# Performance work log

Hardware: AMD Instinct MI355X
Metric: run time of the kernel (lower is better)

The kernel has to match this reference:

```python
import jax, jax.numpy as jnp
import numpy as np

# MLA dims (DeepSeek-V3-lite style)
B, S, DIM = 1, 2048, 2048
H, NOPE, ROPE, VD, LORA = 16, 128, 64, 128, 512
QK_HEAD = NOPE + ROPE  # 192
SCALE = QK_HEAD ** -0.5
EPS = 1e-6


def _rmsnorm(x, w):
    return x * jax.lax.rsqrt(jnp.mean(x * x, axis=-1, keepdims=True) + EPS) * w


def _apply_rope(x, cos, sin):
    # x: [b, s, h, d] with interleaved (real, imag) pairs; cos/sin: [s, d//2]
    x0, x1 = x[..., 0::2], x[..., 1::2]
    c = cos[None, :, None, :]
    s = sin[None, :, None, :]
    y0 = x0 * c - x1 * s
    y1 = x0 * s + x1 * c
    return jnp.stack([y0, y1], axis=-1).reshape(x.shape)


def setup_inputs() -> dict:
    key = jax.random.key(0)
    ks = jax.random.split(key, 6)
    x = jax.random.normal(ks[0], (B, S, DIM), jnp.float32) * 0.02
    wq = jax.random.normal(ks[1], (H * QK_HEAD, DIM), jnp.float32) * 0.02
    wkv_a = jax.random.normal(ks[2], (LORA + ROPE, DIM), jnp.float32) * 0.02
    kv_norm_w = jnp.ones((LORA,), jnp.float32)
    wkv_b = jax.random.normal(ks[3], (H * (NOPE + VD), LORA), jnp.float32) * 0.02
    wo = jax.random.normal(ks[4], (DIM, H * VD), jnp.float32) * 0.02
    # rotary freqs_cis (cos/sin) for qk_rope_head_dim
    inv_freq = 1.0 / (10000.0 ** (np.arange(0, ROPE, 2, dtype=np.float32) / ROPE))
    t = np.arange(S, dtype=np.float32)
    ang = np.outer(t, inv_freq)  # [S, ROPE//2]
    cos = jnp.asarray(np.cos(ang), jnp.float32)
    sin = jnp.asarray(np.sin(ang), jnp.float32)
    return {"x": x, "cos": cos, "sin": sin, "wq": wq, "wkv_a": wkv_a,
            "kv_norm_w": kv_norm_w, "wkv_b": wkv_b, "wo": wo}


def reference(x, cos, sin, wq, wkv_a, kv_norm_w, wkv_b, wo):
    b, s, _ = x.shape
    # queries
    q = (x @ wq.T).reshape(b, s, H, QK_HEAD)
    q_nope, q_pe = q[..., :NOPE], q[..., NOPE:]
    q_pe = _apply_rope(q_pe, cos, sin)  # [b,s,h,rope]
    # latent kv
    kv = x @ wkv_a.T  # [b,s,lora+rope]
    kv_c, k_pe = kv[..., :LORA], kv[..., LORA:]
    k_pe = _apply_rope(k_pe[:, :, None, :], cos, sin)[:, :, 0, :]  # [b,s,rope]
    kv_c = _rmsnorm(kv_c, kv_norm_w)  # latent kv cache [b,s,lora]
    # absorbed weights: wkv_b viewed as [h, nope+vd, lora]
    wkv_b_r = wkv_b.reshape(H, NOPE + VD, LORA)
    w_uk = wkv_b_r[:, :NOPE]   # [h, nope, lora]
    w_uv = wkv_b_r[:, NOPE:]   # [h, vd, lora]
    # absorb: project q_nope into latent space
    q_c = jnp.einsum('bshd,hdc->bshc', q_nope, w_uk)  # [b,s,h,lora]
    scores = (jnp.einsum('bshc,btc->bsht', q_c, kv_c)
              + jnp.einsum('bshr,btr->bsht', q_pe, k_pe)) * SCALE
    # causal mask over [s, t]
    mask = jnp.where(jnp.arange(s)[:, None] >= jnp.arange(s)[None, :], 0.0, -1e30)
    scores = scores + mask[None, :, None, :].astype(scores.dtype)
    attn = jax.nn.softmax(scores, axis=-1)
    o = jnp.einsum('bsht,btc->bshc', attn, kv_c)       # [b,s,h,lora]
    o = jnp.einsum('bshc,hdc->bshd', o, w_uv)           # [b,s,h,vd]
    out = o.reshape(b, s, H * VD) @ wo.T                # [b,s,dim]
    return out
```

## Files before the change

### kernel.cpp

```cpp
#include <hip/hip_runtime.h>
#include <hip/hip_bf16.h>
#include <math.h>

#define S_LEN 2048
#define DIM   2048
#define H_N   16
#define NOPE  128
#define ROPE  64
#define VD    128
#define LORA  512
#define D_QK  576
#define SCALE_F 0.07216878364870323f
#define EPS_F 1e-6f
#define KVF 640
#define KVS 1280

typedef short short8 __attribute__((ext_vector_type(8)));
typedef short short4v __attribute__((ext_vector_type(4)));
typedef float floatx4 __attribute__((ext_vector_type(4)));

static __device__ inline unsigned short f2bf_bits(float f) {
  union { __hip_bfloat16 h; unsigned short u; } cv;
  cv.h = __float2bfloat16(f);
  return cv.u;
}

static __device__ inline float bf2f(unsigned short b) {
  union { unsigned u; float f; } cv;
  cv.u = (unsigned)b << 16;
  return cv.f;
}

static __device__ inline void gload_lds16(const short* gptr, short* lds_base_uniform) {
  __builtin_amdgcn_global_load_lds(
      (const __attribute__((address_space(1))) void*)gptr,
      (__attribute__((address_space(3))) void*)lds_base_uniform, 16, 0, 0);
}

__global__ __launch_bounds__(256) void cast_f32_bf16(
    const float* __restrict__ src, short* __restrict__ dst, int n8) {
  int i = blockIdx.x * 256 + threadIdx.x;
  if (i < n8) {
    float4 a = ((const float4*)src)[2 * i];
    float4 b = ((const float4*)src)[2 * i + 1];
    uint4 o;
    o.x = (unsigned)f2bf_bits(a.x) | ((unsigned)f2bf_bits(a.y) << 16);
    o.y = (unsigned)f2bf_bits(a.z) | ((unsigned)f2bf_bits(a.w) << 16);
    o.z = (unsigned)f2bf_bits(b.x) | ((unsigned)f2bf_bits(b.y) << 16);
    o.w = (unsigned)f2bf_bits(b.z) | ((unsigned)f2bf_bits(b.w) << 16);
    ((uint4*)dst)[i] = o;
  }
}

__global__ __launch_bounds__(256) void zero_short8(short* __restrict__ dst, int n8) {
  int i = blockIdx.x * 256 + threadIdx.x;
  if (i < n8) ((uint4*)dst)[i] = (uint4){0u, 0u, 0u, 0u};
}

__global__ __launch_bounds__(256) void transpose_wuk(
    const float* __restrict__ wkvb, short* __restrict__ wukT) {
  __shared__ float tile[32][33];
  const int h = blockIdx.z, c0 = blockIdx.y * 32, d0 = blockIdx.x * 32;
  const int t = threadIdx.x;
  const int r = t >> 3, c4 = (t & 7) * 4;
  float4 v = *(const float4*)(wkvb + ((long)h * 256 + d0 + r) * 512 + c0 + c4);
  tile[r][c4 + 0] = v.x; tile[r][c4 + 1] = v.y;
  tile[r][c4 + 2] = v.z; tile[r][c4 + 3] = v.w;
  __syncthreads();
  uint2 o;
  o.x = (unsigned)f2bf_bits(tile[c4 + 0][r]) | ((unsigned)f2bf_bits(tile[c4 + 1][r]) << 16);
  o.y = (unsigned)f2bf_bits(tile[c4 + 2][r]) | ((unsigned)f2bf_bits(tile[c4 + 3][r]) << 16);
  *(uint2*)(wukT + ((long)h * 512 + c0 + r) * 128 + d0 + c4) = o;
}

__global__ __launch_bounds__(256) void gemm_bf16_nt(
    const short* __restrict__ A, const short* __restrict__ B, void* __restrict__ Cv,
    int K, int lda, int ldb, int ldc, long aB, long bB, long cB, int bf16out) {
  A += (long)blockIdx.z * aB;
  B += (long)blockIdx.z * bB;
  const int m0 = blockIdx.y * 128, n0 = blockIdx.x * 128;
  __shared__ short As[2][128 * 32];
  __shared__ short Bs[2][128 * 32];
  const int tid = threadIdx.x, w = tid >> 6, lane = tid & 63;
  const int ln = lane & 15, g = lane >> 4;
  const int mw = (w & 1) * 64, nw = (w >> 1) * 64;
  floatx4 acc[4][4];
#pragma unroll
  for (int i = 0; i < 4; ++i)
#pragma unroll
    for (int j = 0; j < 4; ++j) acc[i][j] = (floatx4){0.f, 0.f, 0.f, 0.f};

#define GEMM_STAGE(k0_, b_)                                                    \
  {                                                                            \
    _Pragma("unroll")                                                          \
    for (int i = 0; i < 2; ++i) {                                              \
      const int bc = (i * 4 + w) * 64;                                         \
      const int c = bc + lane;                                                 \
      const int row = c >> 2, quar = c & 3;                                    \
      gload_lds16(A + (long)(m0 + row) * lda + (k0_) + quar * 8, As[b_] + bc * 8); \
      gload_lds16(B + (long)(n0 + row) * ldb + (k0_) + quar * 8, Bs[b_] + bc * 8); \
    }                                                                          \
  }

  GEMM_STAGE(0, 0);
  __syncthreads();
  const int nk = K >> 5;
  for (int kt = 0; kt < nk; ++kt) {
    const int cb = kt & 1;
    if (kt + 1 < nk) GEMM_STAGE((kt + 1) << 5, cb ^ 1);
    short8 af[4], bf_[4];
#pragma unroll
    for (int mi = 0; mi < 4; ++mi)
      af[mi] = *(const short8*)(As[cb] + (mw + mi * 16 + ln) * 32 + g * 8);
#pragma unroll
    for (int ni = 0; ni < 4; ++ni)
      bf_[ni] = *(const short8*)(Bs[cb] + (nw + ni * 16 + ln) * 32 + g * 8);
#pragma unroll
    for (int mi = 0; mi < 4; ++mi)
#pragma unroll
      for (int ni = 0; ni < 4; ++ni)
        acc[mi][ni] = __builtin_amdgcn_mfma_f32_16x16x32_bf16(af[mi], bf_[ni], acc[mi][ni], 0, 0, 0);
    __syncthreads();
  }
#undef GEMM_STAGE
  if (bf16out) {
    short* Cs = (short*)Cv + (long)blockIdx.z * cB;
#pragma unroll
    for (int mi = 0; mi < 4; ++mi)
#pragma unroll
      for (int ni = 0; ni < 4; ++ni)
#pragma unroll
        for (int r = 0; r < 4; ++r)
          Cs[(long)(m0 + mw + mi * 16 + g * 4 + r) * ldc + n0 + nw + ni * 16 + ln] =
              (short)f2bf_bits(acc[mi][ni][r]);
  } else {
    float* C = (float*)Cv + (long)blockIdx.z * cB;
#pragma unroll
    for (int mi = 0; mi < 4; ++mi)
#pragma unroll
      for (int ni = 0; ni < 4; ++ni)
#pragma unroll
        for (int r = 0; r < 4; ++r)
          C[(long)(m0 + mw + mi * 16 + g * 4 + r) * ldc + n0 + nw + ni * 16 + ln] = acc[mi][ni][r];
  }
}

__global__ __launch_bounds__(64) void prep_kernel(
    float* kv, const short* __restrict__ qbufb, short* __restrict__ qhatb,
    const float* __restrict__ cosp, const float* __restrict__ sinp,
    const float* __restrict__ normw) {
  const int s = blockIdx.x;
  const int l = threadIdx.x;
  float* row = kv + (long)s * KVF;
  short* krow = (short*)kv + (long)s * KVS;

  float4 v0 = *(const float4*)(row + l * 8);
  float4 v1 = *(const float4*)(row + l * 8 + 4);
  float rx0 = 0.f, rx1 = 0.f, rc = 0.f, rs = 0.f;
  if (l < 32) {
    rc = cosp[s * 32 + l];
    rs = sinp[s * 32 + l];
    rx0 = row[512 + 2 * l];
    rx1 = row[512 + 2 * l + 1];
  }
  float4 w0 = *(const float4*)(normw + l * 8);
  float4 w1 = *(const float4*)(normw + l * 8 + 4);

  float ss = v0.x * v0.x + v0.y * v0.y + v0.z * v0.z + v0.w * v0.w +
             v1.x * v1.x + v1.y * v1.y + v1.z * v1.z + v1.w * v1.w;
#pragma unroll
  for (int off = 32; off; off >>= 1) ss += __shfl_xor(ss, off, 64);
  const float scale = rsqrtf(ss * (1.0f / (float)LORA) + EPS_F);
  v0.x *= scale * w0.x; v0.y *= scale * w0.y; v0.z *= scale * w0.z; v0.w *= scale * w0.w;
  v1.x *= scale * w1.x; v1.y *= scale * w1.y; v1.z *= scale * w1.z; v1.w *= scale * w1.w;

  uint4 pk;
  pk.x = (unsigned)f2bf_bits(v0.x) | ((unsigned)f2bf_bits(v0.y) << 16);
  pk.y = (unsigned)f2bf_bits(v0.z) | ((unsigned)f2bf_bits(v0.w) << 16);
  pk.z = (unsigned)f2bf_bits(v1.x) | ((unsigned)f2bf_bits(v1.y) << 16);
  pk.w = (unsigned)f2bf_bits(v1.z) | ((unsigned)f2bf_bits(v1.w) << 16);
  *(uint4*)(krow + l * 8) = pk;

  if (l < 32) {
    const float y0 = rx0 * rc - rx1 * rs;
    const float y1 = rx0 * rs + rx1 * rc;
    unsigned pr = (unsigned)f2bf_bits(y0) | ((unsigned)f2bf_bits(y1) << 16);
    *(unsigned*)(krow + 512 + 2 * l) = pr;
  }

#pragma unroll
  for (int it = 0; it < 8; ++it) {
    const int p = it * 64 + l;
    const int h = p >> 5;
    const int i = p & 31;
    const float c = cosp[s * 32 + i];
    const float sn = sinp[s * 32 + i];
    const short* qp = qbufb + (long)s * 3072 + h * 192 + NOPE;
    const unsigned uq = *(const unsigned*)(qp + 2 * i);
    const float x0 = bf2f((unsigned short)uq);
    const float x1 = bf2f((unsigned short)(uq >> 16));
    const float y0 = x0 * c - x1 * sn;
    const float y1 = x0 * sn + x1 * c;
    short* dst = qhatb + ((long)h * S_LEN + s) * D_QK + 512;
    *(unsigned*)(dst + 2 * i) = (unsigned)f2bf_bits(y0) | ((unsigned)f2bf_bits(y1) << 16);
  }
}

__global__ __launch_bounds__(256) void transpose_v(
    const short* __restrict__ kbf, short* __restrict__ kvt) {
  __shared__ short tile[32][36];
  const int d0 = blockIdx.x * 32;
  const int s0 = blockIdx.y * 32;
  const int t = threadIdx.x;
  const int r = t >> 3;
  const int c4 = (t & 7) * 4;
  uint2 v = *(const uint2*)(kbf + (long)(s0 + r) * KVS + d0 + c4);
  *(uint2*)(&tile[r][c4]) = v;
  __syncthreads();
  uint2 o;
  o.x = (unsigned)(unsigned short)tile[c4 + 0][r] | ((unsigned)(unsigned short)tile[c4 + 1][r] << 16);
  o.y = (unsigned)(unsigned short)tile[c4 + 2][r] | ((unsigned)(unsigned short)tile[c4 + 3][r] << 16);
  *(uint2*)(kvt + (long)(d0 + r) * S_LEN + s0 + c4) = o;
}

__global__ __launch_bounds__(256) void build_ktt(
    const short* __restrict__ kbf, short* __restrict__ ktt) {
  const int kt = blockIdx.x;
  for (int idx = threadIdx.x; idx < 18 * 64; idx += 256) {
    const int c = idx >> 6, l = idx & 63;
    const int ln = l & 15, g = l >> 4;
    uint4 v = *(const uint4*)(kbf + (long)(kt * 16 + ln) * KVS + c * 32 + g * 8);
    *(uint4*)(ktt + ((long)(kt * 18 + c) * 64 + l) * 8) = v;
  }
}

__global__ __launch_bounds__(256) void build_vtt(
    const short* __restrict__ kvt, short* __restrict__ vtt) {
  const int kt = blockIdx.x;
  for (int idx = threadIdx.x; idx < 32 * 64; idx += 256) {
    const int nt = idx >> 6, l = idx & 63;
    const int ln = l & 15, g = l >> 4;
    uint4 v = *(const uint4*)(kvt + (long)(nt * 16 + ln) * S_LEN + kt * 32 + g * 8);
    *(uint4*)(vtt + ((long)(kt * 32 + nt) * 64 + l) * 8) = v;
  }
}

__global__ __launch_bounds__(256, 2) void flash_reg(
    const short* __restrict__ qhat,
    const short* __restrict__ ktt,
    const short* __restrict__ vtt,
    short* __restrict__ obuf) {
  const int bid = blockIdx.x;
  const int hp = bid & 7;
  const int v = bid >> 3;
  const int vi = v & 31, vj = v >> 5;
  const int qw = (vj == 0) ? 127 - vi : (vj == 1) ? 64 + vi : (vj == 2) ? 63 - vi : vi;
  const int q0 = qw * 16;
  const int tid = threadIdx.x;
  const int w = tid >> 6;
  const int lane = tid & 63;
  const int ln = lane & 15, g = lane >> 4;
  const int h = hp * 2 + (w & 1);
  const int dh = w >> 1;
  const int vbase = dh * 256;
  const int qlim = q0 + ln;

  __shared__ short Kt[2][36 * 64 * 8];

  short8 qfr[18];
  {
    const short* qrow = qhat + ((long)h * S_LEN + q0 + ln) * D_QK;
#pragma unroll
    for (int c = 0; c < 18; ++c)
      qfr[c] = *(const short8*)(qrow + c * 32 + g * 8);
  }

  floatx4 oacc[16];
#pragma unroll
  for (int nt = 0; nt < 16; ++nt) oacc[nt] = (floatx4){0.f, 0.f, 0.f, 0.f};
  float lsum = 0.f;

  const int npairs = (qw + 2) >> 1;

#define FL_STAGE(pair_, b_)                                                    \
  {                                                                            \
    const short* ksrc_ = ktt + (long)(pair_) * (36 * 512);                     \
    _Pragma("unroll")                                                          \
    for (int i = 0; i < 9; ++i) {                                              \
      const int grp = i * 4 + w;                                               \
      gload_lds16(ksrc_ + (long)(grp * 64 + lane) * 8, Kt[b_] + grp * 512);    \
    }                                                                          \
  }

  FL_STAGE(0, 0);
  __syncthreads();

  for (int p = 0; p < npairs; ++p) {
    const int cb = p & 1;
    if (p + 1 < npairs) FL_STAGE(p + 1, cb ^ 1);
    const int t0 = p * 32;
    const short* kbA = Kt[cb];
    const short* kbB = Kt[cb] + 18 * 512;
    floatx4 sA0 = (floatx4){0.f, 0.f, 0.f, 0.f};
    floatx4 sA1 = (floatx4){0.f, 0.f, 0.f, 0.f};
    floatx4 sB0 = (floatx4){0.f, 0.f, 0.f, 0.f};
    floatx4 sB1 = (floatx4){0.f, 0.f, 0.f, 0.f};
    __builtin_amdgcn_s_setprio(1);
#pragma unroll
    for (int c = 0; c < 18; c += 2) {
      short8 a0 = *(const short8*)(kbA + (c * 64 + lane) * 8);
      short8 a1 = *(const short8*)(kbA + ((c + 1) * 64 + lane) * 8);
      short8 b0 = *(const short8*)(kbB + (c * 64 + lane) * 8);
      short8 b1 = *(const short8*)(kbB + ((c + 1) * 64 + lane) * 8);
      sA0 = __builtin_amdgcn_mfma_f32_16x16x32_bf16(a0, qfr[c], sA0, 0, 0, 0);
      sB0 = __builtin_amdgcn_mfma_f32_16x16x32_bf16(b0, qfr[c], sB0, 0, 0, 0);
      sA1 = __builtin_amdgcn_mfma_f32_16x16x32_bf16(a1, qfr[c + 1], sA1, 0, 0, 0);
      sB1 = __builtin_amdgcn_mfma_f32_16x16x32_bf16(b1, qfr[c + 1], sB1, 0, 0, 0);
    }
    __builtin_amdgcn_s_setprio(0);
    short4v pA4, pB4;
    float psum = 0.f;
#pragma unroll
    for (int r = 0; r < 4; ++r) {
      const int kAi = t0 + g * 4 + r;
      const int kBi = kAi + 16;
      float scA = fminf(fmaxf((sA0[r] + sA1[r]) * SCALE_F, -30.f), 30.f);
      float scB = fminf(fmaxf((sB0[r] + sB1[r]) * SCALE_F, -30.f), 30.f);
      float pA = (kAi <= qlim) ? __expf(scA) : 0.f;
      float pB = (kBi <= qlim) ? __expf(scB) : 0.f;
      psum += pA + pB;
      pA4[r] = (short)f2bf_bits(pA);
      pB4[r] = (short)f2bf_bits(pB);
    }
    lsum += psum;
    union { short4v s; int i[2]; } ua, ub;
    ua.s = pA4; ub.s = pB4;
    const int lolane = ln + ((g & 1) << 5);
    const int hilane = lolane + 16;
    int alo0 = __shfl(ua.i[0], lolane, 64), alo1 = __shfl(ua.i[1], lolane, 64);
    int ahi0 = __shfl(ua.i[0], hilane, 64), ahi1 = __shfl(ua.i[1], hilane, 64);
    int blo0 = __shfl(ub.i[0], lolane, 64), blo1 = __shfl(ub.i[1], lolane, 64);
    int bhi0 = __shfl(ub.i[0], hilane, 64), bhi1 = __shfl(ub.i[1], hilane, 64);
    union { short8 s; int i[4]; } up;
    const bool useA = (g < 2);
    up.i[0] = useA ? alo0 : blo0;
    up.i[1] = useA ? alo1 : blo1;
    up.i[2] = useA ? ahi0 : bhi0;
    up.i[3] = useA ? ahi1 : bhi1;
    const short8 pb8 = up.s;
    const short* vp = vtt + (((long)p * 32 + dh * 16) * 64 + lane) * 8;
#pragma unroll
    for (int half = 0; half < 2; ++half) {
      short8 va[8];
#pragma unroll
      for (int j = 0; j < 8; ++j)
        va[j] = *(const short8*)(vp + (half * 8 + j) * 512);
      __builtin_amdgcn_s_setprio(1);
#pragma unroll
      for (int j = 0; j < 8; ++j)
        oacc[half * 8 + j] = __builtin_amdgcn_mfma_f32_16x16x32_bf16(va[j], pb8, oacc[half * 8 + j], 0, 0, 0);
      __builtin_amdgcn_s_setprio(0);
    }
    __syncthreads();
  }
#undef FL_STAGE

  lsum += __shfl_xor(lsum, 16, 64);
  lsum += __shfl_xor(lsum, 32, 64);
  const float inv = 1.0f / fmaxf(lsum, 1e-30f);

  short* orow = obuf + ((long)h * S_LEN + q0 + ln) * 512 + vbase + g * 4;
#pragma unroll
  for (int nt = 0; nt < 16; ++nt) {
    unsigned lo = (unsigned)f2bf_bits(oacc[nt][0] * inv) | ((unsigned)f2bf_bits(oacc[nt][1] * inv) << 16);
    unsigned hi = (unsigned)f2bf_bits(oacc[nt][2] * inv) | ((unsigned)f2bf_bits(oacc[nt][3] * inv) << 16);
    unsigned long long st = (unsigned long long)lo | ((unsigned long long)hi << 32);
    *(unsigned long long*)(orow + nt * 16) = st;
  }
}

extern "C" void kernel_launch(void* const* d_in, const int* in_sizes, int n_in,
                              void* d_out, int out_size, void* d_ws, size_t ws_size,
                              hipStream_t stream) {
  (void)in_sizes; (void)n_in; (void)out_size; (void)ws_size;
  const float* x      = (const float*)d_in[0];
  const float* cosp   = (const float*)d_in[1];
  const float* sinp   = (const float*)d_in[2];
  const float* wq     = (const float*)d_in[3];
  const float* wkv_a  = (const float*)d_in[4];
  const float* normw  = (const float*)d_in[5];
  const float* wkv_b  = (const float*)d_in[6];
  const float* wo     = (const float*)d_in[7];
  float* out = (float*)d_out;

  float* ws = (float*)d_ws;
  float* qbufR  = ws;
  float* kvold  = qbufR + (long)S_LEN * 3072;
  float* qhatR  = kvold + (long)S_LEN * D_QK;
  float* obufR  = qhatR + (long)H_N * S_LEN * D_QK;
  float* oprojR = obufR + (long)H_N * S_LEN * LORA;

  float* kvpad = oprojR;
  short* kbf = (short*)kvpad;
  short* wkvap = (short*)kvold;

  short* qbufb = (short*)qbufR;
  short* kvt = qbufb + (long)S_LEN * 3072;
  short* ktt = kvt + (long)512 * S_LEN;
  short* vtt = ktt + (long)128 * 18 * 64 * 8;

  short* qhatb  = (short*)qhatR;
  short* wkvbb  = qhatb + (long)H_N * S_LEN * D_QK;
  short* oprojb = wkvbb + (long)4096 * 512;
  short* wob    = oprojb + (long)2048 * 2048;

  short* xb   = (short*)obufR;
  short* wqb  = xb  + (long)2048 * 2048;
  short* wukT = wqb + (long)3072 * 2048;
  short* obufb = (short*)obufR;

  cast_f32_bf16<<<dim3(2048), 256, 0, stream>>>(x, xb, 2048 * 2048 / 8);
  cast_f32_bf16<<<dim3(3072), 256, 0, stream>>>(wq, wqb, 3072 * 2048 / 8);
  cast_f32_bf16<<<dim3(576), 256, 0, stream>>>(wkv_a, wkvap, 576 * 2048 / 8);
  zero_short8<<<dim3(64), 256, 0, stream>>>(wkvap + 576L * 2048, 64 * 2048 / 8);

  gemm_bf16_nt<<<dim3(3072 / 128, 2048 / 128, 1), 256, 0, stream>>>(
      xb, wqb, qbufb, 2048, 2048, 2048, 3072, 0, 0, 0, 1);

  gemm_bf16_nt<<<dim3(KVF / 128, 2048 / 128, 1), 256, 0, stream>>>(
      xb, wkvap, kvpad, 2048, 2048, 2048, KVF, 0, 0, 0, 0);

  prep_kernel<<<dim3(S_LEN), 64, 0, stream>>>(kvpad, qbufb, qhatb, cosp, sinp, normw);

  transpose_wuk<<<dim3(4, 16, 16), 256, 0, stream>>>(wkv_b, wukT);

  gemm_bf16_nt<<<dim3(512 / 128, 2048 / 128, 16), 256, 0, stream>>>(
      qbufb, wukT, qhatb, 128, 3072, 128, 576,
      192L, 512L * 128, (long)S_LEN * D_QK, 1);

  transpose_v<<<dim3(16, 64), 256, 0, stream>>>(kbf, kvt);
  build_ktt<<<dim3(128), 256, 0, stream>>>(kbf, ktt);
  build_vtt<<<dim3(64), 256, 0, stream>>>(kvt, vtt);

  flash_reg<<<dim3(1024), 256, 0, stream>>>(qhatb, ktt, vtt, obufb);

  cast_f32_bf16<<<dim3(1024), 256, 0, stream>>>(wkv_b, wkvbb, 4096 * 512 / 8);

  gemm_bf16_nt<<<dim3(1, 2048 / 128, 16), 256, 0, stream>>>(
      obufb, wkvbb + 128L * 512, oprojb, 512, 512, 512, 2048,
      (long)S_LEN * 512, 256L * 512, 128L, 1);

  cast_f32_bf16<<<dim3(2048), 256, 0, stream>>>(wo, wob, 2048 * 2048 / 8);
  gemm_bf16_nt<<<dim3(2048 / 128, 2048 / 128, 1), 256, 0, stream>>>(
      oprojb, wob, out, 2048, 2048, 2048, 2048, 0, 0, 0, 0);
}
```

Measured before the change: 462.2 us.

## Split QK score work across wave pairs and share P via LDS with skewed PV

Each wave now computes scores for only its half of the 32-key tile instead of both halves, removing the duplicated QK MFMAs between the two waves sharing a head. The probabilities are exchanged through a small double-buffered LDS array instead of register shuffles. The PV multiply is delayed by one iteration so it consumes the previous tile's P after the barrier. Row sums are combined across the wave pair through LDS at the end. This adds LDS traffic and a final barrier, and keeps the PV step one iteration behind the score step.

```diff
diff --git a/kernel.cpp b/kernel.cpp
--- a/kernel.cpp
+++ b/kernel.cpp
@@ -260,12 +260,15 @@
   const int w = tid >> 6;
   const int lane = tid & 63;
   const int ln = lane & 15, g = lane >> 4;
-  const int h = hp * 2 + (w & 1);
+  const int hh = w & 1;
+  const int h = hp * 2 + hh;
   const int dh = w >> 1;
   const int vbase = dh * 256;
   const int qlim = q0 + ln;
 
   __shared__ short Kt[2][36 * 64 * 8];
+  __shared__ __align__(16) short Pl[2][2][16][40];
+  __shared__ float Ls[4][16];
 
   short8 qfr[18];
   {
@@ -292,6 +295,25 @@
     }                                                                          \
   }
 
+#define FL_PV(pp_, par_)                                                       \
+  {                                                                            \
+    const short8 pb8 = *(const short8*)(&Pl[par_][hh][ln][g * 8]);             \
+    const short* vp = vtt + (((long)(pp_) * 32 + dh * 16) * 64 + lane) * 8;    \
+    _Pragma("unroll")                                                          \
+    for (int half = 0; half < 2; ++half) {                                     \
+      short8 va[8];                                                            \
+      _Pragma("unroll")                                                        \
+      for (int j = 0; j < 8; ++j)                                              \
+        va[j] = *(const short8*)(vp + (half * 8 + j) * 512);                   \
+      __builtin_amdgcn_s_setprio(1);                                           \
+      _Pragma("unroll")                                                        \
+      for (int j = 0; j < 8; ++j)                                              \
+        oacc[half * 8 + j] = __builtin_amdgcn_mfma_f32_16x16x32_bf16(          \
+            va[j], pb8, oacc[half * 8 + j], 0, 0, 0);                          \
+      __builtin_amdgcn_s_setprio(0);                                           \
+    }                                                                          \
+  }
+
   FL_STAGE(0, 0);
   __syncthreads();
 
@@ -299,74 +321,44 @@
     const int cb = p & 1;
     if (p + 1 < npairs) FL_STAGE(p + 1, cb ^ 1);
     const int t0 = p * 32;
-    const short* kbA = Kt[cb];
-    const short* kbB = Kt[cb] + 18 * 512;
-    floatx4 sA0 = (floatx4){0.f, 0.f, 0.f, 0.f};
-    floatx4 sA1 = (floatx4){0.f, 0.f, 0.f, 0.f};
-    floatx4 sB0 = (floatx4){0.f, 0.f, 0.f, 0.f};
-    floatx4 sB1 = (floatx4){0.f, 0.f, 0.f, 0.f};
+    const short* kb = Kt[cb] + dh * (18 * 512);
+    floatx4 s0 = (floatx4){0.f, 0.f, 0.f, 0.f};
+    floatx4 s1 = (floatx4){0.f, 0.f, 0.f, 0.f};
     __builtin_amdgcn_s_setprio(1);
 #pragma unroll
     for (int c = 0; c < 18; c += 2) {
-      short8 a0 = *(const short8*)(kbA + (c * 64 + lane) * 8);
-      short8 a1 = *(const short8*)(kbA + ((c + 1) * 64 + lane) * 8);
-      short8 b0 = *(const short8*)(kbB + (c * 64 + lane) * 8);
-      short8 b1 = *(const short8*)(kbB + ((c + 1) * 64 + lane) * 8);
-      sA0 = __builtin_amdgcn_mfma_f32_16x16x32_bf16(a0, qfr[c], sA0, 0, 0, 0);
-      sB0 = __builtin_amdgcn_mfma_f32_16x16x32_bf16(b0, qfr[c], sB0, 0, 0, 0);
-      sA1 = __builtin_amdgcn_mfma_f32_16x16x32_bf16(a1, qfr[c + 1], sA1, 0, 0, 0);
-      sB1 = __builtin_amdgcn_mfma_f32_16x16x32_bf16(b1, qfr[c + 1], sB1, 0, 0, 0);
+      short8 k0 = *(const short8*)(kb + (c * 64 + lane) * 8);
+      short8 k1 = *(const short8*)(kb + ((c + 1) * 64 + lane) * 8);
+      s0 = __builtin_amdgcn_mfma_f32_16x16x32_bf16(k0, qfr[c], s0, 0, 0, 0);
+      s1 = __builtin_amdgcn_mfma_f32_16x16x32_bf16(k1, qfr[c + 1], s1, 0, 0, 0);
     }
     __builtin_amdgcn_s_setprio(0);
-    short4v pA4, pB4;
+    short4v p4;
     float psum = 0.f;
 #pragma unroll
     for (int r = 0; r < 4; ++r) {
-      const int kAi = t0 + g * 4 + r;
-      const int kBi = kAi + 16;
-      float scA = fminf(fmaxf((sA0[r] + sA1[r]) * SCALE_F, -30.f), 30.f);
-      float scB = fminf(fmaxf((sB0[r] + sB1[r]) * SCALE_F, -30.f), 30.f);
-      float pA = (kAi <= qlim) ? __expf(scA) : 0.f;
-      float pB = (kBi <= qlim) ? __expf(scB) : 0.f;
-      psum += pA + pB;
-      pA4[r] = (short)f2bf_bits(pA);
-      pB4[r] = (short)f2bf_bits(pB);
+      const int ki = t0 + dh * 16 + g * 4 + r;
+      float sc = fminf(fmaxf((s0[r] + s1[r]) * SCALE_F, -30.f), 30.f);
+      float pv_ = (ki <= qlim) ? __expf(sc) : 0.f;
+      psum += pv_;
+      p4[r] = (short)f2bf_bits(pv_);
     }
     lsum += psum;
-    union { short4v s; int i[2]; } ua, ub;
-    ua.s = pA4; ub.s = pB4;
-    const int lolane = ln + ((g & 1) << 5);
-    const int hilane = lolane + 16;
-    int alo0 = __shfl(ua.i[0], lolane, 64), alo1 = __shfl(ua.i[1], lolane, 64);
-    int ahi0 = __shfl(ua.i[0], hilane, 64), ahi1 = __shfl(ua.i[1], hilane, 64);
-    int blo0 = __shfl(ub.i[0], lolane, 64), blo1 = __shfl(ub.i[1], lolane, 64);
-    int bhi0 = __shfl(ub.i[0], hilane, 64), bhi1 = __shfl(ub.i[1], hilane, 64);
-    union { short8 s; int i[4]; } up;
-    const bool useA = (g < 2);
-    up.i[0] = useA ? alo0 : blo0;
-    up.i[1] = useA ? alo1 : blo1;
-    up.i[2] = useA ? ahi0 : bhi0;
-    up.i[3] = useA ? ahi1 : bhi1;
-    const short8 pb8 = up.s;
-    const short* vp = vtt + (((long)p * 32 + dh * 16) * 64 + lane) * 8;
-#pragma unroll
-    for (int half = 0; half < 2; ++half) {
-      short8 va[8];
-#pragma unroll
-      for (int j = 0; j < 8; ++j)
-        va[j] = *(const short8*)(vp + (half * 8 + j) * 512);
-      __builtin_amdgcn_s_setprio(1);
-#pragma unroll
-      for (int j = 0; j < 8; ++j)
-        oacc[half * 8 + j] = __builtin_amdgcn_mfma_f32_16x16x32_bf16(va[j], pb8, oacc[half * 8 + j], 0, 0, 0);
-      __builtin_amdgcn_s_setprio(0);
-    }
+    union { short4v s; unsigned long long u; } upk;
+    upk.s = p4;
+    *(unsigned long long*)(&Pl[cb][hh][ln][dh * 16 + g * 4]) = upk.u;
+    if (p > 0) FL_PV(p - 1, cb ^ 1);
     __syncthreads();
   }
+  FL_PV(npairs - 1, (npairs - 1) & 1);
+#undef FL_PV
 #undef FL_STAGE
 
   lsum += __shfl_xor(lsum, 16, 64);
   lsum += __shfl_xor(lsum, 32, 64);
+  if (g == 0) Ls[w][ln] = lsum;
+  __syncthreads();
+  lsum += Ls[w ^ 2][ln];
   const float inv = 1.0f / fmaxf(lsum, 1e-30f);
 
   short* orow = obuf + ((long)h * S_LEN + q0 + ln) * 512 + vbase + g * 4;
```

After: 452.3 us. 1.02x faster.
